# Performance work log

Hardware: AMD Instinct MI355X
Metric: run time of the kernel (lower is better)

## Reference

```python
import jax, jax.numpy as jnp
import numpy as np
from jax import lax

NS, C_IN, C_FEAT, CROP = 16, 3, 32, 256


def _conv(x, w, b):
    # 3x3 stride-1 'SAME' conv == padding=1 in torch
    y = lax.conv_general_dilated(x, w, (1, 1), 'SAME',
                                 dimension_numbers=('NCHW', 'OIHW', 'NCHW'))
    return y + b[None, :, None, None]


def _lrn(x, size=5, alpha=1e-4, beta=0.75, k=1.0):
    # PyTorch LocalResponseNorm: x / (k + alpha/size * sum_window x^2)^beta
    pad = size // 2
    sq = jnp.pad(x * x, ((0, 0), (pad, pad), (0, 0), (0, 0)))
    c = x.shape[1]
    win = sum(sq[:, i:i + c] for i in range(size))
    return x / (k + (alpha / size) * win) ** beta


def setup_inputs() -> dict:
    key = jax.random.key(0)
    ks = jax.random.split(key, 6)
    s = 0.05
    h = np.hanning(CROP).astype(np.float32)
    cos_window = jnp.asarray(np.outer(h, h))
    return {
        'z': jax.random.normal(ks[0], (NS, C_IN, CROP, CROP), jnp.float32),
        'w1': jax.random.normal(ks[1], (C_FEAT, C_IN, 3, 3), jnp.float32) * s,
        'b1': jax.random.normal(ks[2], (C_FEAT,), jnp.float32) * s,
        'w2': jax.random.normal(ks[3], (C_FEAT, C_FEAT, 3, 3), jnp.float32) * s,
        'b2': jax.random.normal(ks[4], (C_FEAT,), jnp.float32) * s,
        'cos_window': cos_window,
        'wf': jax.random.normal(ks[5], (1, C_FEAT, CROP, CROP // 2 + 1, 2), jnp.float32) * s,
    }


def reference(z, w1, b1, w2, b2, cos_window, wf):
    # feature extractor: conv -> relu -> conv -> LRN
    f = jax.nn.relu(_conv(z, w1, b1))
    f = _lrn(_conv(f, w2, b2))
    f = f * cos_window  # (ns, 32, crop, crop)
    zf = jnp.fft.rfft2(f, axes=(-2, -1))  # (ns, 32, crop, crop//2+1) complex
    # faithful to source: w_star = conj(wf), and the loop always uses w_star[0, 1]
    # (fixed channel 1) multiplied with zf[c, l], accumulated over l. wf is detached.
    wc = lax.stop_gradient(wf[0, 1, :, :, 0] - 1j * wf[0, 1, :, :, 1])
    ftrans = wc[None, None] * jnp.sum(zf, axis=1, keepdims=True)  # (ns,1,crop,crop//2+1)
    response = jnp.fft.irfft2(ftrans, s=(CROP, CROP), axes=(-2, -1))
    return response  # (ns, 1, crop, crop)
```

## Files before the change

### kernel.cpp

```cpp
#include <hip/hip_runtime.h>
#include <math.h>

#define NS   16
#define CIN  3
#define CF   32
#define CROP 256
#define KH   129

typedef _Float16 half8  __attribute__((ext_vector_type(8)));
typedef _Float16 half4v __attribute__((ext_vector_type(4)));
typedef float    f32x4  __attribute__((ext_vector_type(4)));

#define X_OFF 0
#define Z_OFF 21504
#define LDS_BYTES 23904

__device__ __forceinline__ int xaddr(int q, int s) {
    return X_OFF + (q << 6) + ((s ^ ((q >> 1) & 3)) << 4);
}

__device__ __forceinline__ int pi_of(int co) {
    int h = co >> 3, j = co & 7;
    return (j < 4) ? (h * 4 + j) : (16 + h * 4 + j - 4);
}
__device__ __forceinline__ int cinv_of(int p) {
    int h = (p & 15) >> 2;
    int j = (p & 3) + ((p >= 16) ? 4 : 0);
    return h * 8 + j;
}

__global__ __launch_bounds__(256)
void prep(const float* __restrict__ w1, const float* __restrict__ w2,
          _Float16* __restrict__ w1pk, _Float16* __restrict__ w2lin,
          _Float16* __restrict__ TAh, _Float16* __restrict__ TAl,
          _Float16* __restrict__ G1h, _Float16* __restrict__ G1l,
          _Float16* __restrict__ G2h, _Float16* __restrict__ G2l,
          _Float16* __restrict__ G3h, _Float16* __restrict__ G3l,
          _Float16* __restrict__ G4h, _Float16* __restrict__ G4l,
          _Float16* __restrict__ TCh, _Float16* __restrict__ TCl)
{
    const int bid = blockIdx.x, tid = threadIdx.x;

    if (bid >= 268) {
        int base = (bid - 268) * 1024 + tid;
        #pragma unroll
        for (int i = 0; i < 4; ++i) {
            int e = base + i * 256;
            if (e < 9216) {
                int co = e / 288;
                int r  = e - co * 288;
                int ci = r / 9, k9 = r - ci * 9;
                w2lin[(k9 * 32 + pi_of(co)) * 32 + ci] = (_Float16)w2[e];
            } else if (e < 9344) {
                int t = e - 9216;
                int lane = t & 63;
                int p = (t >> 6) * 16 + (lane & 15);
                int c = cinv_of(p);
                #pragma unroll
                for (int j = 0; j < 8; ++j) {
                    int k = ((lane >> 4) << 3) + j;
                    w1pk[t * 8 + j] = (k < 27) ? (_Float16)w1[c * 27 + k]
                                               : (_Float16)0.f;
                }
            }
        }
        return;
    }

    __shared__ float cs[256], sn[256];
    {
        float s, c;
        sincosf(0.02454369260617025967f * (float)tid, &s, &c);
        cs[tid] = c; sn[tid] = s;
    }
    __syncthreads();

    if (bid < 68) {
        int base = bid * 1024 + tid;
        #pragma unroll
        for (int i = 0; i < 4; ++i) {
            int e = base + i * 256;
            if (e >= 69632) break;
            int j = e & 7, lane = (e >> 3) & 63, q = e >> 9;
            int nt = q % 17, ks = q / 17;
            int x = ks * 32 + ((lane >> 4) << 3) + j;
            int c = nt * 16 + (lane & 15);
            float v = 0.f;
            if (c <= 128)                    v =  cs[(x * c) & 255];
            else if (c >= 136 && c <= 264)   v = -sn[(x * (c - 136)) & 255];
            _Float16 h = (_Float16)v; TAh[e] = h; TAl[e] = (_Float16)(v - (float)h);
        }
    } else if (bid < 196) {
        int base = (bid - 68) * 1024 + tid;
        #pragma unroll
        for (int i = 0; i < 4; ++i) {
            int e = base + i * 256;
            int j = e & 7, lane = (e >> 3) & 63, q = e >> 9;
            int nt = q & 15, ks = q >> 4;
            int kk = ks * 32 + ((lane >> 4) << 3) + j;
            int m  = nt * 16 + (lane & 15);
            int y = kk & 255, part = kk >> 8;
            int idx = (y * m) & 255;
            float cv = cs[idx], s = sn[idx];
            float g1 = part ? s  : cv;
            float g2 = part ? cv : -s;
            float g3 = (part ? -s : cv) * (1.f / 256.f);
            float g4 = (part ? cv : s) * (1.f / 256.f);
            _Float16 h;
            h = (_Float16)g1; G1h[e] = h; G1l[e] = (_Float16)(g1 - (float)h);
            h = (_Float16)g2; G2h[e] = h; G2l[e] = (_Float16)(g2 - (float)h);
            h = (_Float16)g3; G3h[e] = h; G3l[e] = (_Float16)(g3 - (float)h);
            h = (_Float16)g4; G4h[e] = h; G4l[e] = (_Float16)(g4 - (float)h);
        }
    } else {
        int base = (bid - 196) * 1024 + tid;
        #pragma unroll
        for (int i = 0; i < 4; ++i) {
            int e = base + i * 256;
            int j = e & 7, lane = (e >> 3) & 63, q = e >> 9;
            int nt = q & 15, ks = q >> 4;
            int kk = ks * 32 + ((lane >> 4) << 3) + j;
            int x  = nt * 16 + (lane & 15);
            int part = (kk >= 144) ? 1 : 0, k = kk - part * 144;
            float v = 0.f;
            if (k <= 128) {
                float w = (k == 0 || k == 128) ? 1.f : 2.f;
                int idx = (k * x) & 255;
                v = (part ? -w * sn[idx] : w * cs[idx]) * (1.f / 256.f);
            }
            _Float16 h = (_Float16)v; TCh[e] = h; TCl[e] = (_Float16)(v - (float)h);
        }
    }
}

__global__ __launch_bounds__(256, 5)
void fused_features(const float* __restrict__ z,
                    const _Float16* __restrict__ w1pk,
                    const float* __restrict__ b1,
                    const _Float16* __restrict__ w2lin,
                    const float* __restrict__ b2,
                    const float* __restrict__ cosw,
                    _Float16* __restrict__ g2h, _Float16* __restrict__ g2l)
{
    __shared__ __align__(16) unsigned char smem[LDS_BYTES];
    _Float16* ztile = (_Float16*)(smem + Z_OFF);

    const int tid  = threadIdx.x;
    const int lane = tid & 63;
    const int wv   = tid >> 6;
    const int l15  = lane & 15;
    const int lhi  = lane >> 4;

    const int n  = blockIdx.z;
    const int bx = blockIdx.x, by = blockIdx.y;
    const int fy0 = by * 16 - 1;
    const int fx0 = bx * 16 - 1;

    const int zy0 = by * 16 - 2;
    const int zx0 = bx * 16 - 2;
    for (int idx = tid; idx < CIN * 400; idx += 256) {
        int ci = idx / 400;
        int r  = idx - ci * 400;
        int yy = r / 20, xx = r - yy * 20;
        int gy = zy0 + yy, gx = zx0 + xx;
        float v = 0.0f;
        if ((unsigned)gy < CROP && (unsigned)gx < CROP)
            v = z[((n * CIN + ci) * CROP + gy) * CROP + gx];
        ztile[idx] = (_Float16)v;
    }

    half8 w1f0 = *(const half8*)(w1pk + lane * 8);
    half8 w1f1 = *(const half8*)(w1pk + 512 + lane * 8);
    float bias1v[2][4], bias2v[2][4];
    #pragma unroll
    for (int cg = 0; cg < 2; ++cg)
        #pragma unroll
        for (int r = 0; r < 4; ++r) {
            bias1v[cg][r] = b1[8 * lhi + 4 * cg + r];
            bias2v[cg][r] = b2[8 * lhi + 4 * cg + r];
        }

    int offs[8];
    #pragma unroll
    for (int j = 0; j < 8; ++j) {
        int k = lhi * 8 + j;
        int ci = k / 9, rr = k - ci * 9;
        int ky = rr / 3, kx = rr - ky * 3;
        offs[j] = (k < 27) ? (ci * 400 + ky * 20 + kx) : 0;
    }
    __syncthreads();

    const f32x4 zero4 = {0.f, 0.f, 0.f, 0.f};
    for (int t = wv; t < 21; t += 4) {
        int qp = t * 16 + l15;
        int qpc = qp < 324 ? qp : 323;
        int y = qpc / 18, x = qpc - y * 18;
        const _Float16* zb = ztile + y * 20 + x;
        half8 bfrag;
        #pragma unroll
        for (int j = 0; j < 8; ++j) bfrag[j] = zb[offs[j]];
        f32x4 d0 = __builtin_amdgcn_mfma_f32_16x16x32_f16(w1f0, bfrag, zero4, 0, 0, 0);
        f32x4 d1 = __builtin_amdgcn_mfma_f32_16x16x32_f16(w1f1, bfrag, zero4, 0, 0, 0);
        int gy = fy0 + y, gx = fx0 + x;
        bool ok = ((unsigned)gy < CROP) && ((unsigned)gx < CROP) && (qp < 324);
        half8 o8;
        #pragma unroll
        for (int r = 0; r < 4; ++r) {
            float v0 = ok ? fmaxf(d0[r] + bias1v[0][r], 0.f) : 0.f;
            float v1 = ok ? fmaxf(d1[r] + bias1v[1][r], 0.f) : 0.f;
            o8[r]     = (_Float16)v0;
            o8[4 + r] = (_Float16)v1;
        }
        *(half8*)(smem + xaddr(qp, lhi)) = o8;
    }
    __syncthreads();

    f32x4 acc[4][2];
    #pragma unroll
    for (int tt = 0; tt < 4; ++tt)
        #pragma unroll
        for (int cg = 0; cg < 2; ++cg)
            #pragma unroll
            for (int r = 0; r < 4; ++r)
                acc[tt][cg][r] = bias2v[cg][r];

    #pragma unroll
    for (int k9 = 0; k9 < 9; ++k9) {
        const int ky = k9 / 3, kx = k9 - 3 * ky;
        half8 af0 = *(const half8*)(w2lin + (k9 * 32 + l15)      * 32 + lhi * 8);
        half8 af1 = *(const half8*)(w2lin + (k9 * 32 + l15 + 16) * 32 + lhi * 8);
        #pragma unroll
        for (int tt = 0; tt < 4; ++tt) {
            int q = (wv * 4 + tt + ky) * 18 + l15 + kx;
            half8 bf = *(const half8*)(smem + xaddr(q, lhi));
            acc[tt][0] = __builtin_amdgcn_mfma_f32_16x16x32_f16(af0, bf, acc[tt][0], 0, 0, 0);
            acc[tt][1] = __builtin_amdgcn_mfma_f32_16x16x32_f16(af1, bf, acc[tt][1], 0, 0, 0);
        }
    }

    const bool bot = (lhi == 0), top = (lhi == 3);
    #pragma unroll
    for (int tt = 0; tt < 4; ++tt) {
        float aA0 = acc[tt][0][0], aA1 = acc[tt][0][1],
              aA2 = acc[tt][0][2], aA3 = acc[tt][0][3];
        float aB0 = acc[tt][1][0], aB1 = acc[tt][1][1],
              aB2 = acc[tt][1][2], aB3 = acc[tt][1][3];
        float sA0 = aA0 * aA0, sA1 = aA1 * aA1, sA2 = aA2 * aA2, sA3 = aA3 * aA3;
        float sB0 = aB0 * aB0, sB1 = aB1 * aB1, sB2 = aB2 * aB2, sB3 = aB3 * aB3;
        int up = (lane + 16) & 63, dn = (lane + 48) & 63;
        float em2 = __shfl(sB2, dn); em2 = bot ? 0.f : em2;
        float em1 = __shfl(sB3, dn); em1 = bot ? 0.f : em1;
        float ep8 = __shfl(sA0, up); ep8 = top ? 0.f : ep8;
        float ep9 = __shfl(sA1, up); ep9 = top ? 0.f : ep9;
        float s = 0.f, win = em2 + em1 + sA0 + sA1 + sA2;
        float t2, f;
        t2 = 2e-5f * win; f = fmaf(t2, fmaf(t2, 0.65625f, -0.75f), 1.0f);
        s = fmaf(aA0, f, s);  win += sA3 - em2;
        t2 = 2e-5f * win; f = fmaf(t2, fmaf(t2, 0.65625f, -0.75f), 1.0f);
        s = fmaf(aA1, f, s);  win += sB0 - em1;
        t2 = 2e-5f * win; f = fmaf(t2, fmaf(t2, 0.65625f, -0.75f), 1.0f);
        s = fmaf(aA2, f, s);  win += sB1 - sA0;
        t2 = 2e-5f * win; f = fmaf(t2, fmaf(t2, 0.65625f, -0.75f), 1.0f);
        s = fmaf(aA3, f, s);  win += sB2 - sA1;
        t2 = 2e-5f * win; f = fmaf(t2, fmaf(t2, 0.65625f, -0.75f), 1.0f);
        s = fmaf(aB0, f, s);  win += sB3 - sA2;
        t2 = 2e-5f * win; f = fmaf(t2, fmaf(t2, 0.65625f, -0.75f), 1.0f);
        s = fmaf(aB1, f, s);  win += ep8 - sA3;
        t2 = 2e-5f * win; f = fmaf(t2, fmaf(t2, 0.65625f, -0.75f), 1.0f);
        s = fmaf(aB2, f, s);  win += ep9 - sB0;
        t2 = 2e-5f * win; f = fmaf(t2, fmaf(t2, 0.65625f, -0.75f), 1.0f);
        s = fmaf(aB3, f, s);
        s += __shfl_xor(s, 16);
        s += __shfl_xor(s, 32);
        if (lhi == 0) {
            int gy = by * 16 + wv * 4 + tt, gx = bx * 16 + l15;
            float val = s * cosw[gy * CROP + gx];
            _Float16 h = (_Float16)val;
            int o = (n * CROP + gy) * CROP + gx;
            g2h[o] = h;
            g2l[o] = (_Float16)(val - (float)h);
        }
    }
}

__global__ __launch_bounds__(256, 2)
void fft_rows(const _Float16* __restrict__ g2h, const _Float16* __restrict__ g2l,
              const _Float16* __restrict__ TAh, const _Float16* __restrict__ TAl,
              _Float16* __restrict__ Zth, _Float16* __restrict__ Ztl)
{
    const int lane = threadIdx.x & 63;
    const int wu = blockIdx.x * 4 + (threadIdx.x >> 6);
    const int mt = wu / 17, nt = wu - mt * 17;
    const int l15 = lane & 15, lhi = lane >> 4;
    const int rowA = mt * 16 + l15;

    f32x4 a0 = {}, a1 = {}, a2 = {};
    #pragma unroll
    for (int ks = 0; ks < 8; ++ks) {
        const int ao = rowA * 256 + ks * 32 + lhi * 8;
        half8 Ah = *(const half8*)(g2h + ao);
        half8 Al = *(const half8*)(g2l + ao);
        const int bo = ((ks * 17 + nt) * 64 + lane) * 8;
        half8 Bh = *(const half8*)(TAh + bo);
        half8 Bl = *(const half8*)(TAl + bo);
        a0 = __builtin_amdgcn_mfma_f32_16x16x32_f16(Ah, Bh, a0, 0, 0, 0);
        a1 = __builtin_amdgcn_mfma_f32_16x16x32_f16(Ah, Bl, a1, 0, 0, 0);
        a2 = __builtin_amdgcn_mfma_f32_16x16x32_f16(Al, Bh, a2, 0, 0, 0);
    }
    f32x4 acc;
    #pragma unroll
    for (int r = 0; r < 4; ++r) acc[r] = a0[r] + a1[r] + a2[r];

    const int rowD = mt * 16 + lhi * 4;
    const int n = rowD >> 8, y = rowD & 255;
    int c = nt * 16 + l15;
    int row_k = -1, koff = 0;
    if (c <= 128)                  { row_k = c;       koff = 0;   }
    else if (c >= 136 && c <= 264) { row_k = c - 136; koff = 256; }
    if (row_k >= 0) {
        half4v hv, lv;
        #pragma unroll
        for (int r = 0; r < 4; ++r) {
            float v = acc[r];
            _Float16 h = (_Float16)v;
            hv[r] = h; lv[r] = (_Float16)(v - (float)h);
        }
        size_t o = (size_t)(n * 144 + row_k) * 512 + koff + y;
        *(half4v*)(Zth + o) = hv;
        *(half4v*)(Ztl + o) = lv;
    }
}

__global__ __launch_bounds__(256, 2)
void fft_cols_mul(const _Float16* __restrict__ Zth, const _Float16* __restrict__ Ztl,
                  const _Float16* __restrict__ G1h, const _Float16* __restrict__ G1l,
                  const _Float16* __restrict__ G2h, const _Float16* __restrict__ G2l,
                  const float* __restrict__ wf,
                  _Float16* __restrict__ Ph, _Float16* __restrict__ Pl)
{
    const int lane = threadIdx.x & 63;
    const int wu = blockIdx.x * 4 + (threadIdx.x >> 6);
    const int mt = wu >> 4, nt = wu & 15;
    const int l15 = lane & 15, lhi = lane >> 4;
    const int rowA = mt * 16 + l15;

    f32x4 r0 = {}, r1 = {}, r2 = {}, i0 = {}, i1 = {}, i2 = {};
    #pragma unroll
    for (int ks = 0; ks < 16; ++ks) {
        const int ao = rowA * 512 + ks * 32 + lhi * 8;
        half8 Ah = *(const half8*)(Zth + ao);
        half8 Al = *(const half8*)(Ztl + ao);
        const int bo = ((ks * 16 + nt) * 64 + lane) * 8;
        half8 B1h = *(const half8*)(G1h + bo);
        half8 B1l = *(const half8*)(G1l + bo);
        half8 B2h = *(const half8*)(G2h + bo);
        half8 B2l = *(const half8*)(G2l + bo);
        r0 = __builtin_amdgcn_mfma_f32_16x16x32_f16(Ah, B1h, r0, 0, 0, 0);
        r1 = __builtin_amdgcn_mfma_f32_16x16x32_f16(Ah, B1l, r1, 0, 0, 0);
        r2 = __builtin_amdgcn_mfma_f32_16x16x32_f16(Al, B1h, r2, 0, 0, 0);
        i0 = __builtin_amdgcn_mfma_f32_16x16x32_f16(Ah, B2h, i0, 0, 0, 0);
        i1 = __builtin_amdgcn_mfma_f32_16x16x32_f16(Ah, B2l, i1, 0, 0, 0);
        i2 = __builtin_amdgcn_mfma_f32_16x16x32_f16(Al, B2h, i2, 0, 0, 0);
    }
    const int kbase = (mt % 9) * 16 + lhi * 4;
    const int rowP0 = mt * 16 + lhi * 4;
    const int m = nt * 16 + l15;
    const float* wf1 = wf + 256 * 129 * 2;
    #pragma unroll
    for (int r = 0; r < 4; ++r) {
        int k = kbase + r;
        float wr = wf1[(m * 129 + k) * 2 + 0];
        float wi = wf1[(m * 129 + k) * 2 + 1];
        float fr = r0[r] + r1[r] + r2[r];
        float fi = i0[r] + i1[r] + i2[r];
        float pr = wr * fr + wi * fi;
        float pi = wr * fi - wi * fr;
        size_t o = (size_t)(rowP0 + r) * 512 + m;
        _Float16 h;
        h = (_Float16)pr; Ph[o] = h;       Pl[o] = (_Float16)(pr - (float)h);
        h = (_Float16)pi; Ph[o + 256] = h; Pl[o + 256] = (_Float16)(pi - (float)h);
    }
}

__global__ __launch_bounds__(256, 2)
void fft_cols_inv(const _Float16* __restrict__ Ph, const _Float16* __restrict__ Pl,
                  const _Float16* __restrict__ G3h, const _Float16* __restrict__ G3l,
                  const _Float16* __restrict__ G4h, const _Float16* __restrict__ G4l,
                  _Float16* __restrict__ Bth, _Float16* __restrict__ Btl)
{
    const int lane = threadIdx.x & 63;
    const int wu = blockIdx.x * 4 + (threadIdx.x >> 6);
    const int ri = wu & 1;
    const int rest = wu >> 1;
    const int mt = rest >> 4, nt = rest & 15;
    const int l15 = lane & 15, lhi = lane >> 4;
    const int rowA = mt * 16 + l15;

    const _Float16* Bh_t = ri ? G4h : G3h;
    const _Float16* Bl_t = ri ? G4l : G3l;

    f32x4 a0 = {}, a1 = {}, a2 = {};
    #pragma unroll
    for (int ks = 0; ks < 16; ++ks) {
        const int ao = rowA * 512 + ks * 32 + lhi * 8;
        half8 Ah = *(const half8*)(Ph + ao);
        half8 Al = *(const half8*)(Pl + ao);
        const int bo = ((ks * 16 + nt) * 64 + lane) * 8;
        half8 Bh = *(const half8*)(Bh_t + bo);
        half8 Bl = *(const half8*)(Bl_t + bo);
        a0 = __builtin_amdgcn_mfma_f32_16x16x32_f16(Ah, Bh, a0, 0, 0, 0);
        a1 = __builtin_amdgcn_mfma_f32_16x16x32_f16(Ah, Bl, a1, 0, 0, 0);
        a2 = __builtin_amdgcn_mfma_f32_16x16x32_f16(Al, Bh, a2, 0, 0, 0);
    }
    const int n = mt / 9;
    const int kbase = (mt % 9) * 16 + lhi * 4;
    const int y = nt * 16 + l15;
    size_t base = (size_t)(n * 256 + y) * 288 + ri * 144 + kbase;
    half4v hv, lv;
    #pragma unroll
    for (int r = 0; r < 4; ++r) {
        float v = a0[r] + a1[r] + a2[r];
        _Float16 h = (_Float16)v;
        hv[r] = h; lv[r] = (_Float16)(v - (float)h);
    }
    *(half4v*)(Bth + base) = hv;
    *(half4v*)(Btl + base) = lv;
}

__global__ __launch_bounds__(256, 2)
void irfft_rows(const _Float16* __restrict__ Bth, const _Float16* __restrict__ Btl,
                const _Float16* __restrict__ TCh, const _Float16* __restrict__ TCl,
                float* __restrict__ out)
{
    const int lane = threadIdx.x & 63;
    const int wu = blockIdx.x * 4 + (threadIdx.x >> 6);
    const int mt = wu >> 4, nt = wu & 15;
    const int l15 = lane & 15, lhi = lane >> 4;
    const int rowA = mt * 16 + l15;

    f32x4 a0 = {}, a1 = {}, a2 = {};
    #pragma unroll
    for (int ks = 0; ks < 9; ++ks) {
        const int ao = rowA * 288 + ks * 32 + lhi * 8;
        half8 Ah = *(const half8*)(Bth + ao);
        half8 Al = *(const half8*)(Btl + ao);
        const int bo = ((ks * 16 + nt) * 64 + lane) * 8;
        half8 Bh = *(const half8*)(TCh + bo);
        half8 Bl = *(const half8*)(TCl + bo);
        a0 = __builtin_amdgcn_mfma_f32_16x16x32_f16(Ah, Bh, a0, 0, 0, 0);
        a1 = __builtin_amdgcn_mfma_f32_16x16x32_f16(Ah, Bl, a1, 0, 0, 0);
        a2 = __builtin_amdgcn_mfma_f32_16x16x32_f16(Al, Bh, a2, 0, 0, 0);
    }
    const int rowD = mt * 16 + lhi * 4;
    const int x = nt * 16 + l15;
    #pragma unroll
    for (int r = 0; r < 4; ++r)
        out[(size_t)(rowD + r) * 256 + x] = a0[r] + a1[r] + a2[r];
}

extern "C" void kernel_launch(void* const* d_in, const int* in_sizes, int n_in,
                              void* d_out, int out_size, void* d_ws, size_t ws_size,
                              hipStream_t stream)
{
    const float* z    = (const float*)d_in[0];
    const float* w1   = (const float*)d_in[1];
    const float* b1   = (const float*)d_in[2];
    const float* w2   = (const float*)d_in[3];
    const float* b2   = (const float*)d_in[4];
    const float* cosw = (const float*)d_in[5];
    const float* wf   = (const float*)d_in[6];
    float* out = (float*)d_out;

    char* p = (char*)d_ws;
    auto take = [&](size_t bytes) {
        char* r = p; p += (bytes + 255) & ~(size_t)255; return r;
    };
    _Float16* g2h = (_Float16*)take(4096 * 256 * 2);
    _Float16* g2l = (_Float16*)take(4096 * 256 * 2);
    _Float16* Zth = (_Float16*)take(2304 * 512 * 2);
    _Float16* Ztl = (_Float16*)take(2304 * 512 * 2);
    _Float16* Ph  = (_Float16*)take(2304 * 512 * 2);
    _Float16* Pl  = (_Float16*)take(2304 * 512 * 2);
    _Float16* TAh = (_Float16*)take(69632 * 2);
    _Float16* TAl = (_Float16*)take(69632 * 2);
    _Float16* G1h = (_Float16*)take(131072 * 2);
    _Float16* G1l = (_Float16*)take(131072 * 2);
    _Float16* G2h = (_Float16*)take(131072 * 2);
    _Float16* G2l = (_Float16*)take(131072 * 2);
    _Float16* G3h = (_Float16*)take(131072 * 2);
    _Float16* G3l = (_Float16*)take(131072 * 2);
    _Float16* G4h = (_Float16*)take(131072 * 2);
    _Float16* G4l = (_Float16*)take(131072 * 2);
    _Float16* TCh = (_Float16*)take(73728 * 2);
    _Float16* TCl = (_Float16*)take(73728 * 2);
    _Float16* w1pk  = (_Float16*)take(1024 * 2);
    _Float16* w2lin = (_Float16*)take(9216 * 2);
    _Float16* Bth = Zth;
    _Float16* Btl = Ztl;

    prep<<<278, 256, 0, stream>>>(w1, w2, w1pk, w2lin, TAh, TAl,
                                  G1h, G1l, G2h, G2l, G3h, G3l, G4h, G4l, TCh, TCl);
    fused_features<<<dim3(16, 16, NS), 256, 0, stream>>>(z, w1pk, b1, w2lin, b2,
                                                         cosw, g2h, g2l);
    fft_rows<<<1088, 256, 0, stream>>>(g2h, g2l, TAh, TAl, Zth, Ztl);
    fft_cols_mul<<<576, 256, 0, stream>>>(Zth, Ztl, G1h, G1l, G2h, G2l, wf, Ph, Pl);
    fft_cols_inv<<<1152, 256, 0, stream>>>(Ph, Pl, G3h, G3l, G4h, G4l, Bth, Btl);
    irfft_rows<<<1024, 256, 0, stream>>>(Bth, Btl, TCh, TCl, out);
}
```

Measured before the change: 115.4 us.

## Compute two row tiles per wave in DFT GEMMs and vectorize prep stores

Each wave in the four DFT-as-GEMM kernels now accumulates two 16-row output tiles, so every B-operand (twiddle) fragment load is reused across two MFMA sets. The launch grids are halved and occupancy hints raised. fft_cols_inv also merges its real and imaginary halves into one wave, so the A operand is reused across both twiddle matrices. The prep kernel writes half2 pairs with fewer, larger blocks. This cuts global load traffic per MFMA but doubles accumulator registers and reduces the number of waves.

```diff
diff --git a/kernel.cpp b/kernel.cpp
--- a/kernel.cpp
+++ b/kernel.cpp
@@ -9,6 +9,7 @@
 
 typedef _Float16 half8  __attribute__((ext_vector_type(8)));
 typedef _Float16 half4v __attribute__((ext_vector_type(4)));
+typedef _Float16 half2v __attribute__((ext_vector_type(2)));
 typedef float    f32x4  __attribute__((ext_vector_type(4)));
 
 #define X_OFF 0
@@ -27,6 +28,13 @@
     int h = (p & 15) >> 2;
     int j = (p & 3) + ((p >= 16) ? 4 : 0);
     return h * 8 + j;
+}
+
+__device__ __forceinline__ void split_pair(float v0, float v1,
+                                           half2v* hp, half2v* lp) {
+    _Float16 h0 = (_Float16)v0, h1 = (_Float16)v1;
+    *hp = (half2v){h0, h1};
+    *lp = (half2v){(_Float16)(v0 - (float)h0), (_Float16)(v1 - (float)h1)};
 }
 
 __global__ __launch_bounds__(256)
@@ -41,11 +49,11 @@
 {
     const int bid = blockIdx.x, tid = threadIdx.x;
 
-    if (bid >= 268) {
-        int base = (bid - 268) * 1024 + tid;
-        #pragma unroll
-        for (int i = 0; i < 4; ++i) {
-            int e = base + i * 256;
+    if (bid >= 67) {
+        int base = (bid - 67) * 4096;
+        #pragma unroll
+        for (int i = 0; i < 16; ++i) {
+            int e = base + tid + i * 256;
             if (e < 9216) {
                 int co = e / 288;
                 int r  = e - co * 288;
@@ -75,60 +83,81 @@
     }
     __syncthreads();
 
-    if (bid < 68) {
-        int base = bid * 1024 + tid;
-        #pragma unroll
-        for (int i = 0; i < 4; ++i) {
-            int e = base + i * 256;
-            if (e >= 69632) break;
-            int j = e & 7, lane = (e >> 3) & 63, q = e >> 9;
+    if (bid < 17) {
+        int base = bid * 2048 + tid;
+        #pragma unroll
+        for (int i = 0; i < 8; ++i) {
+            int p = base + i * 256;
+            int j0 = (p & 3) * 2, lane = (p >> 2) & 63, q = p >> 8;
             int nt = q % 17, ks = q / 17;
-            int x = ks * 32 + ((lane >> 4) << 3) + j;
+            int x0 = ks * 32 + ((lane >> 4) << 3) + j0;
             int c = nt * 16 + (lane & 15);
-            float v = 0.f;
-            if (c <= 128)                    v =  cs[(x * c) & 255];
-            else if (c >= 136 && c <= 264)   v = -sn[(x * (c - 136)) & 255];
-            _Float16 h = (_Float16)v; TAh[e] = h; TAl[e] = (_Float16)(v - (float)h);
-        }
-    } else if (bid < 196) {
-        int base = (bid - 68) * 1024 + tid;
-        #pragma unroll
-        for (int i = 0; i < 4; ++i) {
-            int e = base + i * 256;
-            int j = e & 7, lane = (e >> 3) & 63, q = e >> 9;
+            float v0 = 0.f, v1 = 0.f;
+            if (c <= 128) {
+                v0 =  cs[(x0 * c) & 255];
+                v1 =  cs[((x0 + 1) * c) & 255];
+            } else if (c >= 136 && c <= 264) {
+                int cc = c - 136;
+                v0 = -sn[(x0 * cc) & 255];
+                v1 = -sn[((x0 + 1) * cc) & 255];
+            }
+            half2v hv, lv; split_pair(v0, v1, &hv, &lv);
+            ((half2v*)TAh)[p] = hv; ((half2v*)TAl)[p] = lv;
+        }
+    } else if (bid < 49) {
+        int base = (bid - 17) * 2048 + tid;
+        #pragma unroll
+        for (int i = 0; i < 8; ++i) {
+            int p = base + i * 256;
+            int j0 = (p & 3) * 2, lane = (p >> 2) & 63, q = p >> 8;
             int nt = q & 15, ks = q >> 4;
-            int kk = ks * 32 + ((lane >> 4) << 3) + j;
+            int kk0 = ks * 32 + ((lane >> 4) << 3) + j0;
             int m  = nt * 16 + (lane & 15);
-            int y = kk & 255, part = kk >> 8;
-            int idx = (y * m) & 255;
-            float cv = cs[idx], s = sn[idx];
-            float g1 = part ? s  : cv;
-            float g2 = part ? cv : -s;
-            float g3 = (part ? -s : cv) * (1.f / 256.f);
-            float g4 = (part ? cv : s) * (1.f / 256.f);
-            _Float16 h;
-            h = (_Float16)g1; G1h[e] = h; G1l[e] = (_Float16)(g1 - (float)h);
-            h = (_Float16)g2; G2h[e] = h; G2l[e] = (_Float16)(g2 - (float)h);
-            h = (_Float16)g3; G3h[e] = h; G3l[e] = (_Float16)(g3 - (float)h);
-            h = (_Float16)g4; G4h[e] = h; G4l[e] = (_Float16)(g4 - (float)h);
+            int part = kk0 >> 8;
+            int y0 = kk0 & 255;
+            int i0 = (y0 * m) & 255, i1 = ((y0 + 1) * m) & 255;
+            float cv0 = cs[i0], s0 = sn[i0], cv1 = cs[i1], s1 = sn[i1];
+            half2v hv, lv;
+            float a0 = part ? s0 : cv0,  a1 = part ? s1 : cv1;
+            split_pair(a0, a1, &hv, &lv);
+            ((half2v*)G1h)[p] = hv; ((half2v*)G1l)[p] = lv;
+            a0 = part ? cv0 : -s0;  a1 = part ? cv1 : -s1;
+            split_pair(a0, a1, &hv, &lv);
+            ((half2v*)G2h)[p] = hv; ((half2v*)G2l)[p] = lv;
+            a0 = (part ? -s0 : cv0) * (1.f/256.f);
+            a1 = (part ? -s1 : cv1) * (1.f/256.f);
+            split_pair(a0, a1, &hv, &lv);
+            ((half2v*)G3h)[p] = hv; ((half2v*)G3l)[p] = lv;
+            a0 = (part ? cv0 : s0) * (1.f/256.f);
+            a1 = (part ? cv1 : s1) * (1.f/256.f);
+            split_pair(a0, a1, &hv, &lv);
+            ((half2v*)G4h)[p] = hv; ((half2v*)G4l)[p] = lv;
         }
     } else {
-        int base = (bid - 196) * 1024 + tid;
-        #pragma unroll
-        for (int i = 0; i < 4; ++i) {
-            int e = base + i * 256;
-            int j = e & 7, lane = (e >> 3) & 63, q = e >> 9;
+        int base = (bid - 49) * 2048 + tid;
+        #pragma unroll
+        for (int i = 0; i < 8; ++i) {
+            int p = base + i * 256;
+            int j0 = (p & 3) * 2, lane = (p >> 2) & 63, q = p >> 8;
             int nt = q & 15, ks = q >> 4;
-            int kk = ks * 32 + ((lane >> 4) << 3) + j;
+            int kk0 = ks * 32 + ((lane >> 4) << 3) + j0;
             int x  = nt * 16 + (lane & 15);
-            int part = (kk >= 144) ? 1 : 0, k = kk - part * 144;
-            float v = 0.f;
-            if (k <= 128) {
-                float w = (k == 0 || k == 128) ? 1.f : 2.f;
-                int idx = (k * x) & 255;
-                v = (part ? -w * sn[idx] : w * cs[idx]) * (1.f / 256.f);
+            int part = (kk0 >= 144) ? 1 : 0;
+            int k0 = kk0 - part * 144;
+            float v0 = 0.f, v1 = 0.f;
+            if (k0 <= 128) {
+                float w0 = (k0 == 0 || k0 == 128) ? 1.f : 2.f;
+                int ii = (k0 * x) & 255;
+                v0 = (part ? -w0 * sn[ii] : w0 * cs[ii]) * (1.f/256.f);
             }
-            _Float16 h = (_Float16)v; TCh[e] = h; TCl[e] = (_Float16)(v - (float)h);
+            int k1 = k0 + 1;
+            if (k1 <= 128) {
+                float w1w = (k1 == 0 || k1 == 128) ? 1.f : 2.f;
+                int ii = (k1 * x) & 255;
+                v1 = (part ? -w1w * sn[ii] : w1w * cs[ii]) * (1.f/256.f);
+            }
+            half2v hv, lv; split_pair(v0, v1, &hv, &lv);
+            ((half2v*)TCh)[p] = hv; ((half2v*)TCl)[p] = lv;
         }
     }
 }
@@ -283,51 +312,52 @@
     }
 }
 
-__global__ __launch_bounds__(256, 2)
+__global__ __launch_bounds__(256, 4)
 void fft_rows(const _Float16* __restrict__ g2h, const _Float16* __restrict__ g2l,
               const _Float16* __restrict__ TAh, const _Float16* __restrict__ TAl,
               _Float16* __restrict__ Zth, _Float16* __restrict__ Ztl)
 {
     const int lane = threadIdx.x & 63;
     const int wu = blockIdx.x * 4 + (threadIdx.x >> 6);
-    const int mt = wu / 17, nt = wu - mt * 17;
+    const int mt2 = wu / 17, nt = wu - mt2 * 17;
     const int l15 = lane & 15, lhi = lane >> 4;
-    const int rowA = mt * 16 + l15;
-
-    f32x4 a0 = {}, a1 = {}, a2 = {};
+
+    f32x4 a[2][3] = {};
     #pragma unroll
     for (int ks = 0; ks < 8; ++ks) {
-        const int ao = rowA * 256 + ks * 32 + lhi * 8;
-        half8 Ah = *(const half8*)(g2h + ao);
-        half8 Al = *(const half8*)(g2l + ao);
         const int bo = ((ks * 17 + nt) * 64 + lane) * 8;
         half8 Bh = *(const half8*)(TAh + bo);
         half8 Bl = *(const half8*)(TAl + bo);
-        a0 = __builtin_amdgcn_mfma_f32_16x16x32_f16(Ah, Bh, a0, 0, 0, 0);
-        a1 = __builtin_amdgcn_mfma_f32_16x16x32_f16(Ah, Bl, a1, 0, 0, 0);
-        a2 = __builtin_amdgcn_mfma_f32_16x16x32_f16(Al, Bh, a2, 0, 0, 0);
-    }
-    f32x4 acc;
-    #pragma unroll
-    for (int r = 0; r < 4; ++r) acc[r] = a0[r] + a1[r] + a2[r];
-
-    const int rowD = mt * 16 + lhi * 4;
-    const int n = rowD >> 8, y = rowD & 255;
+        #pragma unroll
+        for (int rt = 0; rt < 2; ++rt) {
+            const int ao = (mt2 * 32 + rt * 16 + l15) * 256 + ks * 32 + lhi * 8;
+            half8 Ah = *(const half8*)(g2h + ao);
+            half8 Al = *(const half8*)(g2l + ao);
+            a[rt][0] = __builtin_amdgcn_mfma_f32_16x16x32_f16(Ah, Bh, a[rt][0], 0, 0, 0);
+            a[rt][1] = __builtin_amdgcn_mfma_f32_16x16x32_f16(Ah, Bl, a[rt][1], 0, 0, 0);
+            a[rt][2] = __builtin_amdgcn_mfma_f32_16x16x32_f16(Al, Bh, a[rt][2], 0, 0, 0);
+        }
+    }
     int c = nt * 16 + l15;
     int row_k = -1, koff = 0;
     if (c <= 128)                  { row_k = c;       koff = 0;   }
     else if (c >= 136 && c <= 264) { row_k = c - 136; koff = 256; }
     if (row_k >= 0) {
-        half4v hv, lv;
-        #pragma unroll
-        for (int r = 0; r < 4; ++r) {
-            float v = acc[r];
-            _Float16 h = (_Float16)v;
-            hv[r] = h; lv[r] = (_Float16)(v - (float)h);
-        }
-        size_t o = (size_t)(n * 144 + row_k) * 512 + koff + y;
-        *(half4v*)(Zth + o) = hv;
-        *(half4v*)(Ztl + o) = lv;
+        #pragma unroll
+        for (int rt = 0; rt < 2; ++rt) {
+            const int rowD = mt2 * 32 + rt * 16 + lhi * 4;
+            const int n = rowD >> 8, y = rowD & 255;
+            half4v hv, lv;
+            #pragma unroll
+            for (int r = 0; r < 4; ++r) {
+                float v = a[rt][0][r] + a[rt][1][r] + a[rt][2][r];
+                _Float16 h = (_Float16)v;
+                hv[r] = h; lv[r] = (_Float16)(v - (float)h);
+            }
+            size_t o = (size_t)(n * 144 + row_k) * 512 + koff + y;
+            *(half4v*)(Zth + o) = hv;
+            *(half4v*)(Ztl + o) = lv;
+        }
     }
 }
 
@@ -340,45 +370,51 @@
 {
     const int lane = threadIdx.x & 63;
     const int wu = blockIdx.x * 4 + (threadIdx.x >> 6);
-    const int mt = wu >> 4, nt = wu & 15;
+    const int mt2 = wu >> 4, nt = wu & 15;
     const int l15 = lane & 15, lhi = lane >> 4;
-    const int rowA = mt * 16 + l15;
-
-    f32x4 r0 = {}, r1 = {}, r2 = {}, i0 = {}, i1 = {}, i2 = {};
+
+    f32x4 rr[2][3] = {}, ii[2][3] = {};
     #pragma unroll
     for (int ks = 0; ks < 16; ++ks) {
-        const int ao = rowA * 512 + ks * 32 + lhi * 8;
-        half8 Ah = *(const half8*)(Zth + ao);
-        half8 Al = *(const half8*)(Ztl + ao);
         const int bo = ((ks * 16 + nt) * 64 + lane) * 8;
         half8 B1h = *(const half8*)(G1h + bo);
         half8 B1l = *(const half8*)(G1l + bo);
         half8 B2h = *(const half8*)(G2h + bo);
         half8 B2l = *(const half8*)(G2l + bo);
-        r0 = __builtin_amdgcn_mfma_f32_16x16x32_f16(Ah, B1h, r0, 0, 0, 0);
-        r1 = __builtin_amdgcn_mfma_f32_16x16x32_f16(Ah, B1l, r1, 0, 0, 0);
-        r2 = __builtin_amdgcn_mfma_f32_16x16x32_f16(Al, B1h, r2, 0, 0, 0);
-        i0 = __builtin_amdgcn_mfma_f32_16x16x32_f16(Ah, B2h, i0, 0, 0, 0);
-        i1 = __builtin_amdgcn_mfma_f32_16x16x32_f16(Ah, B2l, i1, 0, 0, 0);
-        i2 = __builtin_amdgcn_mfma_f32_16x16x32_f16(Al, B2h, i2, 0, 0, 0);
-    }
-    const int kbase = (mt % 9) * 16 + lhi * 4;
-    const int rowP0 = mt * 16 + lhi * 4;
+        #pragma unroll
+        for (int rt = 0; rt < 2; ++rt) {
+            const int ao = (mt2 * 32 + rt * 16 + l15) * 512 + ks * 32 + lhi * 8;
+            half8 Ah = *(const half8*)(Zth + ao);
+            half8 Al = *(const half8*)(Ztl + ao);
+            rr[rt][0] = __builtin_amdgcn_mfma_f32_16x16x32_f16(Ah, B1h, rr[rt][0], 0, 0, 0);
+            rr[rt][1] = __builtin_amdgcn_mfma_f32_16x16x32_f16(Ah, B1l, rr[rt][1], 0, 0, 0);
+            rr[rt][2] = __builtin_amdgcn_mfma_f32_16x16x32_f16(Al, B1h, rr[rt][2], 0, 0, 0);
+            ii[rt][0] = __builtin_amdgcn_mfma_f32_16x16x32_f16(Ah, B2h, ii[rt][0], 0, 0, 0);
+            ii[rt][1] = __builtin_amdgcn_mfma_f32_16x16x32_f16(Ah, B2l, ii[rt][1], 0, 0, 0);
+            ii[rt][2] = __builtin_amdgcn_mfma_f32_16x16x32_f16(Al, B2h, ii[rt][2], 0, 0, 0);
+        }
+    }
     const int m = nt * 16 + l15;
     const float* wf1 = wf + 256 * 129 * 2;
     #pragma unroll
-    for (int r = 0; r < 4; ++r) {
-        int k = kbase + r;
-        float wr = wf1[(m * 129 + k) * 2 + 0];
-        float wi = wf1[(m * 129 + k) * 2 + 1];
-        float fr = r0[r] + r1[r] + r2[r];
-        float fi = i0[r] + i1[r] + i2[r];
-        float pr = wr * fr + wi * fi;
-        float pi = wr * fi - wi * fr;
-        size_t o = (size_t)(rowP0 + r) * 512 + m;
-        _Float16 h;
-        h = (_Float16)pr; Ph[o] = h;       Pl[o] = (_Float16)(pr - (float)h);
-        h = (_Float16)pi; Ph[o + 256] = h; Pl[o + 256] = (_Float16)(pi - (float)h);
+    for (int rt = 0; rt < 2; ++rt) {
+        const int mtr = mt2 * 2 + rt;
+        const int kbase = (mtr % 9) * 16 + lhi * 4;
+        const int rowP0 = mtr * 16 + lhi * 4;
+        #pragma unroll
+        for (int r = 0; r < 4; ++r) {
+            int k = kbase + r;
+            float wr = wf1[(m * 129 + k) * 2 + 0];
+            float wi = wf1[(m * 129 + k) * 2 + 1];
+            float fr = rr[rt][0][r] + rr[rt][1][r] + rr[rt][2][r];
+            float fi = ii[rt][0][r] + ii[rt][1][r] + ii[rt][2][r];
+            float pr = wr * fr + wi * fi;
+            float pi = wr * fi - wi * fr;
+            size_t o = (size_t)(rowP0 + r) * 512 + m;
+            _Float16 h;
+            h = (_Float16)pr; Ph[o] = h;       Pl[o] = (_Float16)(pr - (float)h);
+            h = (_Float16)pi; Ph[o + 256] = h; Pl[o + 256] = (_Float16)(pi - (float)h);
+        }
     }
 }
 
@@ -390,72 +426,88 @@
 {
     const int lane = threadIdx.x & 63;
     const int wu = blockIdx.x * 4 + (threadIdx.x >> 6);
-    const int ri = wu & 1;
-    const int rest = wu >> 1;
-    const int mt = rest >> 4, nt = rest & 15;
+    const int mt2 = wu >> 4, nt = wu & 15;
     const int l15 = lane & 15, lhi = lane >> 4;
-    const int rowA = mt * 16 + l15;
-
-    const _Float16* Bh_t = ri ? G4h : G3h;
-    const _Float16* Bl_t = ri ? G4l : G3l;
-
-    f32x4 a0 = {}, a1 = {}, a2 = {};
+
+    f32x4 rr[2][3] = {}, ii[2][3] = {};
     #pragma unroll
     for (int ks = 0; ks < 16; ++ks) {
-        const int ao = rowA * 512 + ks * 32 + lhi * 8;
-        half8 Ah = *(const half8*)(Ph + ao);
-        half8 Al = *(const half8*)(Pl + ao);
         const int bo = ((ks * 16 + nt) * 64 + lane) * 8;
-        half8 Bh = *(const half8*)(Bh_t + bo);
-        half8 Bl = *(const half8*)(Bl_t + bo);
-        a0 = __builtin_amdgcn_mfma_f32_16x16x32_f16(Ah, Bh, a0, 0, 0, 0);
-        a1 = __builtin_amdgcn_mfma_f32_16x16x32_f16(Ah, Bl, a1, 0, 0, 0);
-        a2 = __builtin_amdgcn_mfma_f32_16x16x32_f16(Al, Bh, a2, 0, 0, 0);
-    }
-    const int n = mt / 9;
-    const int kbase = (mt % 9) * 16 + lhi * 4;
+        half8 B3h = *(const half8*)(G3h + bo);
+        half8 B3l = *(const half8*)(G3l + bo);
+        half8 B4h = *(const half8*)(G4h + bo);
+        half8 B4l = *(const half8*)(G4l + bo);
+        #pragma unroll
+        for (int rt = 0; rt < 2; ++rt) {
+            const int ao = (mt2 * 32 + rt * 16 + l15) * 512 + ks * 32 + lhi * 8;
+            half8 Ah = *(const half8*)(Ph + ao);
+            half8 Al = *(const half8*)(Pl + ao);
+            rr[rt][0] = __builtin_amdgcn_mfma_f32_16x16x32_f16(Ah, B3h, rr[rt][0], 0, 0, 0);
+            rr[rt][1] = __builtin_amdgcn_mfma_f32_16x16x32_f16(Ah, B3l, rr[rt][1], 0, 0, 0);
+            rr[rt][2] = __builtin_amdgcn_mfma_f32_16x16x32_f16(Al, B3h, rr[rt][2], 0, 0, 0);
+            ii[rt][0] = __builtin_amdgcn_mfma_f32_16x16x32_f16(Ah, B4h, ii[rt][0], 0, 0, 0);
+            ii[rt][1] = __builtin_amdgcn_mfma_f32_16x16x32_f16(Ah, B4l, ii[rt][1], 0, 0, 0);
+            ii[rt][2] = __builtin_amdgcn_mfma_f32_16x16x32_f16(Al, B4h, ii[rt][2], 0, 0, 0);
+        }
+    }
     const int y = nt * 16 + l15;
-    size_t base = (size_t)(n * 256 + y) * 288 + ri * 144 + kbase;
-    half4v hv, lv;
-    #pragma unroll
-    for (int r = 0; r < 4; ++r) {
-        float v = a0[r] + a1[r] + a2[r];
-        _Float16 h = (_Float16)v;
-        hv[r] = h; lv[r] = (_Float16)(v - (float)h);
-    }
-    *(half4v*)(Bth + base) = hv;
-    *(half4v*)(Btl + base) = lv;
-}
-
-__global__ __launch_bounds__(256, 2)
+    #pragma unroll
+    for (int rt = 0; rt < 2; ++rt) {
+        const int mtr = mt2 * 2 + rt;
+        const int n = mtr / 9;
+        const int kbase = (mtr % 9) * 16 + lhi * 4;
+        size_t base = (size_t)(n * 256 + y) * 288 + kbase;
+        half4v hv0, lv0, hv1, lv1;
+        #pragma unroll
+        for (int r = 0; r < 4; ++r) {
+            float v = rr[rt][0][r] + rr[rt][1][r] + rr[rt][2][r];
+            _Float16 h = (_Float16)v;
+            hv0[r] = h; lv0[r] = (_Float16)(v - (float)h);
+            float v2 = ii[rt][0][r] + ii[rt][1][r] + ii[rt][2][r];
+            _Float16 h2 = (_Float16)v2;
+            hv1[r] = h2; lv1[r] = (_Float16)(v2 - (float)h2);
+        }
+        *(half4v*)(Bth + base) = hv0;
+        *(half4v*)(Btl + base) = lv0;
+        *(half4v*)(Bth + base + 144) = hv1;
+        *(half4v*)(Btl + base + 144) = lv1;
+    }
+}
+
+__global__ __launch_bounds__(256, 4)
 void irfft_rows(const _Float16* __restrict__ Bth, const _Float16* __restrict__ Btl,
                 const _Float16* __restrict__ TCh, const _Float16* __restrict__ TCl,
                 float* __restrict__ out)
 {
     const int lane = threadIdx.x & 63;
     const int wu = blockIdx.x * 4 + (threadIdx.x >> 6);
-    const int mt = wu >> 4, nt = wu & 15;
+    const int mt2 = wu >> 4, nt = wu & 15;
     const int l15 = lane & 15, lhi = lane >> 4;
-    const int rowA = mt * 16 + l15;
-
-    f32x4 a0 = {}, a1 = {}, a2 = {};
+
+    f32x4 a[2][3] = {};
     #pragma unroll
     for (int ks = 0; ks < 9; ++ks) {
-        const int ao = rowA * 288 + ks * 32 + lhi * 8;
-        half8 Ah = *(const half8*)(Bth + ao);
-        half8 Al = *(const half8*)(Btl + ao);
         const int bo = ((ks * 16 + nt) * 64 + lane) * 8;
         half8 Bh = *(const half8*)(TCh + bo);
         half8 Bl = *(const half8*)(TCl + bo);
-        a0 = __builtin_amdgcn_mfma_f32_16x16x32_f16(Ah, Bh, a0, 0, 0, 0);
-        a1 = __builtin_amdgcn_mfma_f32_16x16x32_f16(Ah, Bl, a1, 0, 0, 0);
-        a2 = __builtin_amdgcn_mfma_f32_16x16x32_f16(Al, Bh, a2, 0, 0, 0);
-    }
-    const int rowD = mt * 16 + lhi * 4;
+        #pragma unroll
+        for (int rt = 0; rt < 2; ++rt) {
+            const int ao = (mt2 * 32 + rt * 16 + l15) * 288 + ks * 32 + lhi * 8;
+            half8 Ah = *(const half8*)(Bth + ao);
+            half8 Al = *(const half8*)(Btl + ao);
+            a[rt][0] = __builtin_amdgcn_mfma_f32_16x16x32_f16(Ah, Bh, a[rt][0], 0, 0, 0);
+            a[rt][1] = __builtin_amdgcn_mfma_f32_16x16x32_f16(Ah, Bl, a[rt][1], 0, 0, 0);
+            a[rt][2] = __builtin_amdgcn_mfma_f32_16x16x32_f16(Al, Bh, a[rt][2], 0, 0, 0);
+        }
+    }
     const int x = nt * 16 + l15;
     #pragma unroll
-    for (int r = 0; r < 4; ++r)
-        out[(size_t)(rowD + r) * 256 + x] = a0[r] + a1[r] + a2[r];
+    for (int rt = 0; rt < 2; ++rt) {
+        const int rowD = mt2 * 32 + rt * 16 + lhi * 4;
+        #pragma unroll
+        for (int r = 0; r < 4; ++r)
+            out[(size_t)(rowD + r) * 256 + x] = a[rt][0][r] + a[rt][1][r] + a[rt][2][r];
+    }
 }
 
 extern "C" void kernel_launch(void* const* d_in, const int* in_sizes, int n_in,
@@ -498,12 +550,12 @@
     _Float16* Bth = Zth;
     _Float16* Btl = Ztl;
 
-    prep<<<278, 256, 0, stream>>>(w1, w2, w1pk, w2lin, TAh, TAl,
-                                  G1h, G1l, G2h, G2l, G3h, G3l, G4h, G4l, TCh, TCl);
+    prep<<<70, 256, 0, stream>>>(w1, w2, w1pk, w2lin, TAh, TAl,
+                                 G1h, G1l, G2h, G2l, G3h, G3l, G4h, G4l, TCh, TCl);
     fused_features<<<dim3(16, 16, NS), 256, 0, stream>>>(z, w1pk, b1, w2lin, b2,
                                                          cosw, g2h, g2l);
-    fft_rows<<<1088, 256, 0, stream>>>(g2h, g2l, TAh, TAl, Zth, Ztl);
-    fft_cols_mul<<<576, 256, 0, stream>>>(Zth, Ztl, G1h, G1l, G2h, G2l, wf, Ph, Pl);
-    fft_cols_inv<<<1152, 256, 0, stream>>>(Ph, Pl, G3h, G3l, G4h, G4l, Bth, Btl);
-    irfft_rows<<<1024, 256, 0, stream>>>(Bth, Btl, TCh, TCl, out);
-}
+    fft_rows<<<544, 256, 0, stream>>>(g2h, g2l, TAh, TAl, Zth, Ztl);
+    fft_cols_mul<<<288, 256, 0, stream>>>(Zth, Ztl, G1h, G1l, G2h, G2l, wf, Ph, Pl);
+    fft_cols_inv<<<288, 256, 0, stream>>>(Ph, Pl, G3h, G3l, G4h, G4l, Bth, Btl);
+    irfft_rows<<<512, 256, 0, stream>>>(Bth, Btl, TCh, TCl, out);
+}
```

Result: slower. 119.9 us (+3.9%).
